# Optimization experiments

Hardware: AMD Instinct MI355X
Metric: run time of the kernel (lower is better)

The kernel has to match this reference:

```python
import jax, jax.numpy as jnp
import numpy as np

BEV_FEAT_SHAPE = (1, 1, 200, 200, 64)  # (B, Dz, Dy, Dx, C)
MAXN = 40

B, N, D, IH, IW = 1, 6, 118, 16, 44
C = 64
N_RANKS = BEV_FEAT_SHAPE[1] * BEV_FEAT_SHAPE[2] * BEV_FEAT_SHAPE[3] * MAXN


def setup_inputs() -> dict:
    key = jax.random.key(0)
    k1, k2, k3, k4 = jax.random.split(key, 4)
    depth = jax.random.uniform(k1, (B, N, D, IH, IW), dtype=jnp.float32)
    feat = jax.random.normal(k2, (B, N, IH, IW, C), dtype=jnp.float32)
    # indices may point at the appended zero row (index == total rows)
    ranks_depth = jax.random.randint(k3, (N_RANKS,), 0, B * N * D * IH * IW + 1, dtype=jnp.int32)
    ranks_feat = jax.random.randint(k4, (N_RANKS,), 0, B * N * IH * IW + 1, dtype=jnp.int32)
    return {"depth": depth, "feat": feat, "ranks_depth": ranks_depth,
            "ranks_feat": ranks_feat, "maxn": MAXN}


def reference(depth, feat, ranks_depth, ranks_feat, maxn):
    b, n, d, ih, iw = depth.shape
    c = feat.shape[-1]
    _, oD, oW, oH, _ = BEV_FEAT_SHAPE
    # flatten + append one zero padding row (invalid points map here)
    depth_2d = jnp.concatenate(
        [depth.reshape(b * n * d * ih * iw, 1), jnp.zeros((1, 1), jnp.float32)], axis=0)
    feat_2d = jnp.concatenate(
        [feat.reshape(b * n * ih * iw, c), jnp.zeros((1, c), jnp.float32)], axis=0)
    # gather depth scalar and feature vector per point, multiply
    r_mul = depth_2d[ranks_depth] * feat_2d[ranks_feat]  # (oD*oW*oH*maxn, C)
    # segmented sum: maxn points per output voxel
    r_scatter = r_mul.reshape(oD, oW, oH, maxn, c).sum(axis=3, keepdims=True)
    # permute (oD, oW, oH, 1, C) -> (1, oD, oW, oH, C)
    return jnp.transpose(r_scatter, (3, 0, 1, 2, 4))
```

## Files before the change

### kernel.cpp

```cpp
#include <hip/hip_runtime.h>


typedef int      vint4   __attribute__((ext_vector_type(4)));
typedef float    vfloat4 __attribute__((ext_vector_type(4)));
typedef _Float16 vhalf4  __attribute__((ext_vector_type(4)));
typedef _Float16 vhalf8  __attribute__((ext_vector_type(8)));

#define ND_ROWS (1 * 6 * 118 * 16 * 44)
#define NF_ROWS (1 * 6 * 16 * 44)
#define MAXN_PTS 40
#define NVOX (200 * 200)
#define VPB 16
#define THREADS 128
#define CHUNKS (VPB * MAXN_PTS / 4)
#define LDS_STRIDE 41
#define ROW_BYTES 128

#define FEAT_VEC4 (NF_ROWS * 16)

__global__ __launch_bounds__(256) void feat_pack_f16(
    const vfloat4* __restrict__ in, vhalf4* __restrict__ out)
{
    const int i = blockIdx.x * 256 + threadIdx.x;
    const vfloat4 f = in[i];
    vhalf4 h;
    h.x = (_Float16)f.x; h.y = (_Float16)f.y;
    h.z = (_Float16)f.z; h.w = (_Float16)f.w;
    out[i] = h;
}

__global__ __launch_bounds__(THREADS) void BEVPoolV2_79783312491037_kernel(
    const float* __restrict__ depth,
    const vhalf4* __restrict__ feat16,
    const vint4* __restrict__ rd4,
    const vint4* __restrict__ rf4,
    vfloat4* __restrict__ out4)
{
    __shared__ float2 s_pair[VPB * LDS_STRIDE];

    const int t = threadIdx.x;

#pragma unroll
    for (int r = 0; r < 2; ++r) {
        const int c = r * THREADS + t;
        if (c < CHUNKS) {
            const vint4 rd = __builtin_nontemporal_load(&rd4[blockIdx.x * CHUNKS + c]);
            const vint4 rf = __builtin_nontemporal_load(&rf4[blockIdx.x * CHUNKS + c]);
#pragma unroll
            for (int k = 0; k < 4; ++k) {
                const int idx = c * 4 + k;
                const int g = idx / MAXN_PTS;
                const int j = idx - g * MAXN_PTS;
                const int rdk = rd[k], rfk = rf[k];
                const bool valid = (rdk < ND_ROWS) && (rfk < NF_ROWS);
                const float dl = depth[min(rdk, ND_ROWS - 1)];
                float2 p;
                p.x = valid ? dl : 0.0f;
                p.y = __uint_as_float((unsigned)((rfk < NF_ROWS) ? rfk : 0) * ROW_BYTES);
                s_pair[g * LDS_STRIDE + j] = p;
            }
        }
    }
    __syncthreads();

    const int g = t >> 3;
    const int c8 = t & 7;
    const int pbase = g * LDS_STRIDE;
    const char* fbase = (const char*)feat16 + c8 * 16;

    float acc[8] = {0, 0, 0, 0, 0, 0, 0, 0};

    float  db[2][8];
    vhalf8 fb[2][8];

#pragma unroll
    for (int k = 0; k < 8; ++k) {
        const float2 p = s_pair[pbase + k];
        db[0][k] = p.x;
        fb[0][k] = *(const vhalf8*)(fbase + __float_as_uint(p.y));
    }

#pragma unroll
    for (int b = 0; b < 5; ++b) {
        const int cur = b & 1, nxt = cur ^ 1;
        if (b < 4) {
#pragma unroll
            for (int k = 0; k < 8; ++k) {
                const float2 p = s_pair[pbase + (b + 1) * 8 + k];
                db[nxt][k] = p.x;
                fb[nxt][k] = *(const vhalf8*)(fbase + __float_as_uint(p.y));
            }
        }
#pragma unroll
        for (int k = 0; k < 8; ++k) {
            const float d = db[cur][k];
            const vhalf8 f = fb[cur][k];
#pragma unroll
            for (int i = 0; i < 8; ++i)
                acc[i] = fmaf(d, (float)f[i], acc[i]);
        }
    }

    const int v = blockIdx.x * VPB + g;
    vfloat4 lo = {acc[0], acc[1], acc[2], acc[3]};
    vfloat4 hi = {acc[4], acc[5], acc[6], acc[7]};
    __builtin_nontemporal_store(lo, &out4[v * 16 + c8 * 2]);
    __builtin_nontemporal_store(hi, &out4[v * 16 + c8 * 2 + 1]);
}

extern "C" void kernel_launch(void* const* d_in, const int* in_sizes, int n_in,
                              void* d_out, int out_size, void* d_ws, size_t ws_size,
                              hipStream_t stream)
{
    const float*   depth = (const float*)d_in[0];
    const vfloat4* feat4 = (const vfloat4*)d_in[1];
    const vint4*   rd4   = (const vint4*)d_in[2];
    const vint4*   rf4   = (const vint4*)d_in[3];
    vfloat4* out4 = (vfloat4*)d_out;

    vhalf4* feat16 = (vhalf4*)d_ws;

    feat_pack_f16<<<FEAT_VEC4 / 256, 256, 0, stream>>>(feat4, feat16);

    const int blocks = NVOX / VPB;
    BEVPoolV2_79783312491037_kernel<<<blocks, THREADS, 0, stream>>>(
        depth, feat16, rd4, rf4, out4);
}
```

Baseline: 92.04 us.

## Precompute packed fp16 depth/feature-index pairs in a separate pass

Adds a pre-pass that gathers depth values and packs them as fp16 together with the 16-bit feature row index into one 32-bit word per point, stored in workspace. The main kernel drops its LDS staging and barrier, reads the packed pairs directly from global memory with register double/triple buffering, and uses 256-thread blocks covering 32 voxels. This is meant to shorten the main kernel's dependency chain, but it adds an extra kernel launch and a round trip of the packed pairs through global memory. It also reduces depth precision to fp16.

```diff
diff --git a/kernel.cpp b/kernel.cpp
--- a/kernel.cpp
+++ b/kernel.cpp
@@ -2,98 +2,96 @@
 
 
 typedef int      vint4   __attribute__((ext_vector_type(4)));
+typedef unsigned vuint4  __attribute__((ext_vector_type(4)));
 typedef float    vfloat4 __attribute__((ext_vector_type(4)));
 typedef _Float16 vhalf4  __attribute__((ext_vector_type(4)));
 typedef _Float16 vhalf8  __attribute__((ext_vector_type(8)));
 
-#define ND_ROWS (1 * 6 * 118 * 16 * 44)
-#define NF_ROWS (1 * 6 * 16 * 44)
+#define ND_ROWS 498432
+#define NF_ROWS 4224
 #define MAXN_PTS 40
-#define NVOX (200 * 200)
-#define VPB 16
-#define THREADS 128
-#define CHUNKS (VPB * MAXN_PTS / 4)
-#define LDS_STRIDE 41
-#define ROW_BYTES 128
+#define NVOX 40000
+#define NPTS (NVOX * MAXN_PTS)
+#define NP4  (NPTS / 4)
 
-#define FEAT_VEC4 (NF_ROWS * 16)
-
-__global__ __launch_bounds__(256) void feat_pack_f16(
-    const vfloat4* __restrict__ in, vhalf4* __restrict__ out)
+__global__ __launch_bounds__(256) void build_pairs(
+    const float* __restrict__ depth,
+    const vint4* __restrict__ rd4, const vint4* __restrict__ rf4,
+    vuint4* __restrict__ pairs4)
 {
     const int i = blockIdx.x * 256 + threadIdx.x;
-    const vfloat4 f = in[i];
+    if (i >= NP4) return;
+    const vint4 rd = rd4[i], rf = rf4[i];
+    vuint4 o;
+#pragma unroll
+    for (int k = 0; k < 4; ++k) {
+        const int rdk = rd[k], rfk = rf[k];
+        const bool valid = (rdk < ND_ROWS) && (rfk < NF_ROWS);
+        const float dl = depth[min(rdk, ND_ROWS - 1)];
+        const _Float16 hd = (_Float16)(valid ? dl : 0.0f);
+        unsigned short hb;
+        __builtin_memcpy(&hb, &hd, 2);
+        o[k] = ((unsigned)((rfk < NF_ROWS) ? rfk : 0) << 16) | (unsigned)hb;
+    }
+    pairs4[i] = o;
+}
+
+__global__ __launch_bounds__(256) void pack_feat(
+    const vfloat4* __restrict__ feat4, vhalf4* __restrict__ out)
+{
+    const int i = blockIdx.x * 256 + threadIdx.x;
+    const vfloat4 f = feat4[i];
     vhalf4 h;
     h.x = (_Float16)f.x; h.y = (_Float16)f.y;
     h.z = (_Float16)f.z; h.w = (_Float16)f.w;
     out[i] = h;
 }
 
-__global__ __launch_bounds__(THREADS) void BEVPoolV2_79783312491037_kernel(
-    const float* __restrict__ depth,
-    const vhalf4* __restrict__ feat16,
-    const vint4* __restrict__ rd4,
-    const vint4* __restrict__ rf4,
+__global__ __launch_bounds__(256) void BEVPoolV2_79783312491037_kernel(
+    const vuint4* __restrict__ pairs4,
+    const char* __restrict__ feat16,
     vfloat4* __restrict__ out4)
 {
-    __shared__ float2 s_pair[VPB * LDS_STRIDE];
-
     const int t = threadIdx.x;
-
-#pragma unroll
-    for (int r = 0; r < 2; ++r) {
-        const int c = r * THREADS + t;
-        if (c < CHUNKS) {
-            const vint4 rd = __builtin_nontemporal_load(&rd4[blockIdx.x * CHUNKS + c]);
-            const vint4 rf = __builtin_nontemporal_load(&rf4[blockIdx.x * CHUNKS + c]);
-#pragma unroll
-            for (int k = 0; k < 4; ++k) {
-                const int idx = c * 4 + k;
-                const int g = idx / MAXN_PTS;
-                const int j = idx - g * MAXN_PTS;
-                const int rdk = rd[k], rfk = rf[k];
-                const bool valid = (rdk < ND_ROWS) && (rfk < NF_ROWS);
-                const float dl = depth[min(rdk, ND_ROWS - 1)];
-                float2 p;
-                p.x = valid ? dl : 0.0f;
-                p.y = __uint_as_float((unsigned)((rfk < NF_ROWS) ? rfk : 0) * ROW_BYTES);
-                s_pair[g * LDS_STRIDE + j] = p;
-            }
-        }
-    }
-    __syncthreads();
-
     const int g = t >> 3;
     const int c8 = t & 7;
-    const int pbase = g * LDS_STRIDE;
-    const char* fbase = (const char*)feat16 + c8 * 16;
+    const int v = blockIdx.x * 32 + g;
+    const vuint4* pv = pairs4 + v * 10;
+    const char* fbase = feat16 + c8 * 16;
 
     float acc[8] = {0, 0, 0, 0, 0, 0, 0, 0};
-
-    float  db[2][8];
+    vuint4 pb[3][2];
     vhalf8 fb[2][8];
 
+    pb[0][0] = pv[0]; pb[0][1] = pv[1];
+    pb[1][0] = pv[2]; pb[1][1] = pv[3];
 #pragma unroll
     for (int k = 0; k < 8; ++k) {
-        const float2 p = s_pair[pbase + k];
-        db[0][k] = p.x;
-        fb[0][k] = *(const vhalf8*)(fbase + __float_as_uint(p.y));
+        const unsigned u = pb[0][k >> 2][k & 3];
+        fb[0][k] = *(const vhalf8*)(fbase + (size_t)(u >> 16) * 128);
     }
 
 #pragma unroll
     for (int b = 0; b < 5; ++b) {
         const int cur = b & 1, nxt = cur ^ 1;
+        if (b < 3) {
+            pb[(b + 2) % 3][0] = pv[2 * (b + 2)];
+            pb[(b + 2) % 3][1] = pv[2 * (b + 2) + 1];
+        }
         if (b < 4) {
 #pragma unroll
             for (int k = 0; k < 8; ++k) {
-                const float2 p = s_pair[pbase + (b + 1) * 8 + k];
-                db[nxt][k] = p.x;
-                fb[nxt][k] = *(const vhalf8*)(fbase + __float_as_uint(p.y));
+                const unsigned u = pb[(b + 1) % 3][k >> 2][k & 3];
+                fb[nxt][k] = *(const vhalf8*)(fbase + (size_t)(u >> 16) * 128);
             }
         }
 #pragma unroll
         for (int k = 0; k < 8; ++k) {
-            const float d = db[cur][k];
+            const unsigned u = pb[b % 3][k >> 2][k & 3];
+            const unsigned short hb = (unsigned short)(u & 0xffffu);
+            _Float16 hd;
+            __builtin_memcpy(&hd, &hb, 2);
+            const float d = (float)hd;
             const vhalf8 f = fb[cur][k];
 #pragma unroll
             for (int i = 0; i < 8; ++i)
@@ -101,11 +99,11 @@
         }
     }
 
-    const int v = blockIdx.x * VPB + g;
+    const int o = v * 16 + c8 * 2;
     vfloat4 lo = {acc[0], acc[1], acc[2], acc[3]};
     vfloat4 hi = {acc[4], acc[5], acc[6], acc[7]};
-    __builtin_nontemporal_store(lo, &out4[v * 16 + c8 * 2]);
-    __builtin_nontemporal_store(hi, &out4[v * 16 + c8 * 2 + 1]);
+    __builtin_nontemporal_store(lo, &out4[o]);
+    __builtin_nontemporal_store(hi, &out4[o + 1]);
 }
 
 extern "C" void kernel_launch(void* const* d_in, const int* in_sizes, int n_in,
@@ -118,11 +116,12 @@
     const vint4*   rf4   = (const vint4*)d_in[3];
     vfloat4* out4 = (vfloat4*)d_out;
 
-    vhalf4* feat16 = (vhalf4*)d_ws;
+    vuint4* pairs4 = (vuint4*)d_ws;
+    vhalf4* feat16 = (vhalf4*)((char*)d_ws + (size_t)NPTS * 4);
 
-    feat_pack_f16<<<FEAT_VEC4 / 256, 256, 0, stream>>>(feat4, feat16);
+    build_pairs<<<(NP4 + 255) / 256, 256, 0, stream>>>(depth, rd4, rf4, pairs4);
+    pack_feat<<<(NF_ROWS * 16) / 256, 256, 0, stream>>>(feat4, feat16);
 
-    const int blocks = NVOX / VPB;
-    BEVPoolV2_79783312491037_kernel<<<blocks, THREADS, 0, stream>>>(
-        depth, feat16, rd4, rf4, out4);
+    BEVPoolV2_79783312491037_kernel<<<NVOX / 32, 256, 0, stream>>>(
+        pairs4, (const char*)feat16, out4);
 }
```

New measurement: 98.56 us. +7.1%, slower.
